# Kernel optimization log

Measured on AMD Instinct MI355X. Metric: run time of the kernel, lower is better.

## Reference

```python
import jax, jax.numpy as jnp
import numpy as np

N_NODES = 50000


def gcn_conv(x, W, b, src, dst, n_nodes):
    """PyG-style GCNConv: self-loops + symmetric deg^-1/2 normalization.

    x: [N, Fin], W: [Fin, Fout], b: [Fout], src/dst: [E] int.
    """
    h = x @ W  # [N, Fout] -- transform before aggregation (small GEMM)
    loop = jnp.arange(n_nodes, dtype=src.dtype)
    src2 = jnp.concatenate([src, loop])  # [E+N]
    dst2 = jnp.concatenate([dst, loop])
    # degree on target nodes (all edge weights = 1, includes self loops)
    deg = jax.ops.segment_sum(jnp.ones(src2.shape[0], dtype=h.dtype), dst2,
                              num_segments=n_nodes)
    dinv = jnp.where(deg > 0, jax.lax.rsqrt(deg), 0.0)
    norm = dinv[src2] * dinv[dst2]  # [E+N]
    msg = h[src2] * norm[:, None]   # gather + scale (memory bound)
    out = jax.ops.segment_sum(msg, dst2, num_segments=n_nodes)  # scatter-add
    return out + b


def setup_inputs() -> dict:
    key = jax.random.key(0)
    ks = jax.random.split(key, 8)
    input_dim, hidden_dim, output_dim = 128, 64, 64
    n_edges = 800000
    x = jax.random.normal(ks[0], (N_NODES, input_dim), dtype=jnp.float32)
    edge_index = jax.random.randint(ks[1], (2, n_edges), 0, N_NODES,
                                    dtype=jnp.int32)
    def glorot(k, fan_in, fan_out):
        s = jnp.sqrt(6.0 / (fan_in + fan_out)).astype(jnp.float32)
        return jax.random.uniform(k, (fan_in, fan_out), jnp.float32, -s, s)
    return {
        "x": x,
        "edge_index": edge_index,
        "W1": glorot(ks[2], input_dim, hidden_dim),
        "b1": jnp.zeros((hidden_dim,), jnp.float32),
        "W2": glorot(ks[3], hidden_dim, output_dim),
        "b2": jnp.zeros((output_dim,), jnp.float32),
        "Wfc": glorot(ks[4], output_dim, 1),
        "bfc": jnp.zeros((1,), jnp.float32),
    }


def reference(x, edge_index, W1, b1, W2, b2, Wfc, bfc):
    src, dst = edge_index[0], edge_index[1]
    h = gcn_conv(x, W1, b1, src, dst, N_NODES)
    h = jax.nn.relu(h)
    h = gcn_conv(h, W2, b2, src, dst, N_NODES)
    logits = h @ Wfc + bfc  # [N, 1]
    return jax.nn.sigmoid(logits)
```

## Files before the change

### kernel.cpp

```cpp
#include <hip/hip_runtime.h>
#include <hip/hip_bf16.h>

#define NN 50000
#define FIN 128
#define NT (NN / 16)
#define NREG 196
#define SLAB 8960
#define NBINB 512
#define CAP2 32
#define NGEMB ((NT + 3) / 4)
#define STCAP 5200

typedef unsigned char u8;
typedef unsigned short u16;
typedef unsigned int u32;
typedef __attribute__((ext_vector_type(8))) short short8;
typedef __attribute__((ext_vector_type(4))) float floatx4;

__device__ __forceinline__ float b2f(u16 v) {
  union { u32 u; float f; } x; x.u = ((u32)v) << 16; return x.f;
}
__device__ __forceinline__ u16 f2b(float f) {
  union { u32 u; float f; } x; x.f = f;
  u32 r = x.u + 0x7FFFu + ((x.u >> 16) & 1u);
  return (u16)(r >> 16);
}
__device__ __forceinline__ float lo16(u32 u) {
  union { u32 x; float f; } c; c.x = u << 16; return c.f;
}
__device__ __forceinline__ float hi16(u32 u) {
  union { u32 x; float f; } c; c.x = u & 0xFFFF0000u; return c.f;
}

__global__ __launch_bounds__(256) void k_prep_bin_gemm(
    const u32* __restrict__ xw, int nxw, const void* __restrict__ w1, int n1w,
    const void* __restrict__ w2, int n2w, const void* __restrict__ wf, int nfw,
    const u16* __restrict__ b2, const u16* __restrict__ bfc,
    float* __restrict__ w2f, float* __restrict__ cbias, int* __restrict__ flags,
    const int* __restrict__ src, const int* __restrict__ dst, int E,
    u32* __restrict__ bucket, u8* __restrict__ cntm,
    const void* __restrict__ X, u16* __restrict__ g,
    float* __restrict__ dinv, float* __restrict__ tvec) {
  int t = threadIdx.x;
  int blk = blockIdx.x;
  if (blk >= NGEMB && blk < NGEMB + NBINB) {
    __shared__ int cnt2[NREG];
    for (int i = t; i < NREG; i += 256) cnt2[i] = 0;
    __syncthreads();
    int sl = blk - NGEMB;
    int lo = (int)((long long)sl * E / NBINB);
    int hi = (int)((long long)(sl + 1) * E / NBINB);
    for (int e = lo + t; e < hi; e += 256) {
      int d = dst[e];
      int s = src[e];
      int r = d >> 8;
      int ofs = atomicAdd(&cnt2[r], 1);
      if (ofs < CAP2)
        bucket[((size_t)sl * NREG + r) * CAP2 + ofs] =
            ((u32)(d & 255) << 16) | (u32)s;
    }
    __syncthreads();
    for (int i = t; i < NREG; i += 256) {
      int c = cnt2[i];
      cntm[(size_t)sl * NREG + i] = (u8)(c > CAP2 ? CAP2 : c);
    }
    return;
  }
  if (blk >= NGEMB + NBINB) {
    __shared__ int sc[3];
    if (t < 3) sc[t] = 0;
    __syncthreads();
    const u32* p2 = (const u32*)w2;
    const u32* pf = (const u32*)wf;
    int n2s = n2w < 1024 ? n2w : 1024;
    int nfs = nfw < 1024 ? nfw : 1024;
    int sn = nxw < 1024 ? nxw : 1024;
    int s2 = 0, sf = 0, sx = 0;
    for (int i = t; i < n2s; i += 256) {
      u32 w = p2[i];
      u32 e = (w >> 7) & 0xFFu;
      s2 += (e >= 100u && e <= 132u) ? 1 : -1;
    }
    for (int i = t; i < nfs; i += 256) {
      u32 w = pf[i];
      u32 e = (w >> 7) & 0xFFu;
      sf += (e >= 100u && e <= 132u) ? 1 : -1;
    }
    for (int i = t; i < sn; i += 256) {
      u32 w = xw[i];
      u32 e = (w >> 7) & 0xFFu;
      sx += (e >= 100u && e <= 132u) ? 1 : -1;
    }
    if (s2) atomicAdd(&sc[0], s2);
    if (sf) atomicAdd(&sc[1], sf);
    if (sx) atomicAdd(&sc[2], sx);
    __syncthreads();
    int f2 = sc[0] > 0, f3 = sc[1] > 0;
    if (t == 0) { flags[0] = sc[2] > 0; flags[2] = f2; flags[3] = f3; }
    if (t < 64) {
      float acc = 0.f;
      for (int j = 0; j < 64; ++j) {
        float w2v = f2 ? b2f(((const u16*)w2)[t * 64 + j])
                       : ((const float*)w2)[t * 64 + j];
        float wfv = f3 ? b2f(((const u16*)wf)[j]) : ((const float*)wf)[j];
        acc += w2v * wfv;
      }
      w2f[t] = acc;
    } else if (t == 64) {
      float acc = b2f(bfc[0]);
      for (int j = 0; j < 64; ++j) {
        float wfv = f3 ? b2f(((const u16*)wf)[j]) : ((const float*)wf)[j];
        acc += b2f(b2[j]) * wfv;
      }
      cbias[0] = acc;
    } else if (t >= 128 && t < 192) {
      g[(size_t)NN * 64 + (t - 128)] = 0;
    } else if (t == 192) {
      tvec[NN] = 0.f;
    } else if (t == 193) {
      dinv[NN] = 0.f;
    }
    return;
  }
  __shared__ u16 lwh[FIN * 64];
  __shared__ u16 lwl[FIN * 64];
  __shared__ int scg[2];
  if (t < 2) scg[t] = 0;
  __syncthreads();
  {
    int sn = nxw < 1024 ? nxw : 1024;
    int sx = 0;
    for (int i = t; i < sn; i += 256) {
      u32 w = xw[i];
      u32 e = (w >> 7) & 0xFFu;
      sx += (e >= 100u && e <= 132u) ? 1 : -1;
    }
    if (sx) atomicAdd(&scg[0], sx);
    int s1n = n1w < 1024 ? n1w : 1024;
    const u32* p1 = (const u32*)w1;
    int s1 = 0;
    for (int i = t; i < s1n; i += 256) {
      u32 w = p1[i];
      u32 e = (w >> 7) & 0xFFu;
      s1 += (e >= 100u && e <= 132u) ? 1 : -1;
    }
    if (s1) atomicAdd(&scg[1], s1);
  }
  __syncthreads();
  bool xb = scg[0] > 0;
  bool w1b = scg[1] > 0;
  for (int i = t; i < FIN * 64; i += 256) {
    int j = i & 7, L = (i >> 3) & 63, f = i >> 9;
    int k = (f >> 2) * 32 + (L >> 4) * 8 + j;
    int n = (f & 3) * 16 + (L & 15);
    int idx = k * 64 + n;
    float v = w1b ? b2f(((const u16*)w1)[idx]) : ((const float*)w1)[idx];
    u16 hb = f2b(v);
    lwh[i] = hb;
    lwl[i] = f2b(v - b2f(hb));
  }
  __syncthreads();
  constexpr int KC = FIN / 32;
  int wave = t >> 6, lane = t & 63;
  int rt = blk * 4 + wave;
  if (rt >= NT) return;
  int m = rt * 16 + (lane & 15);
  int q = (lane >> 4) * 8;
  short8 ah[KC], al[KC];
  if (xb) {
    const u16* xr = (const u16*)X + (size_t)m * FIN + q;
#pragma unroll
    for (int kc = 0; kc < KC; ++kc) ah[kc] = *(const short8*)(xr + kc * 32);
  } else {
    const float* xr = (const float*)X + (size_t)m * FIN + q;
#pragma unroll
    for (int kc = 0; kc < KC; ++kc) {
      float4 v0 = *(const float4*)(xr + kc * 32);
      float4 v1 = *(const float4*)(xr + kc * 32 + 4);
      float v[8] = {v0.x, v0.y, v0.z, v0.w, v1.x, v1.y, v1.z, v1.w};
      short8 h8, l8;
#pragma unroll
      for (int j = 0; j < 8; ++j) {
        u16 hb = f2b(v[j]);
        h8[j] = (short)hb;
        l8[j] = (short)f2b(v[j] - b2f(hb));
      }
      ah[kc] = h8;
      al[kc] = l8;
    }
  }
  int row0 = rt * 16 + (lane >> 4) * 4;
  int c0 = lane & 15;
#pragma unroll
  for (int ct = 0; ct < 4; ++ct) {
    short8 bh[KC], bl[KC];
#pragma unroll
    for (int kc = 0; kc < KC; ++kc) {
      int fo = ((kc * 4 + ct) * 64 + lane) * 8;
      bh[kc] = *(const short8*)(lwh + fo);
      bl[kc] = *(const short8*)(lwl + fo);
    }
    floatx4 acc = (floatx4)(0.f);
#pragma unroll
    for (int kc = 0; kc < KC; ++kc) {
      if (!xb)
        acc = __builtin_amdgcn_mfma_f32_16x16x32_bf16(al[kc], bh[kc], acc, 0, 0, 0);
      acc = __builtin_amdgcn_mfma_f32_16x16x32_bf16(ah[kc], bl[kc], acc, 0, 0, 0);
      acc = __builtin_amdgcn_mfma_f32_16x16x32_bf16(ah[kc], bh[kc], acc, 0, 0, 0);
    }
    size_t o = (size_t)row0 * 64 + ct * 16 + c0;
#pragma unroll
    for (int r = 0; r < 4; ++r) g[o + (size_t)r * 64] = f2b(acc[r]);
  }
}

__global__ __launch_bounds__(512) void k_assemble(
    const u32* __restrict__ bucket, const u8* __restrict__ cntm,
    int* __restrict__ rowstart, int* __restrict__ cnt,
    float* __restrict__ dinv, u16* __restrict__ csr) {
  __shared__ u32 stage[STCAP];
  __shared__ int h[256];
  __shared__ int off[256];
  __shared__ int wsum[8];
  __shared__ int nws[4];
  __shared__ int tot_s;
  int r = blockIdx.x, t = threadIdx.x;
  int lane = t & 63, w = t >> 6;
  int c = (int)cntm[(size_t)t * NREG + r];
  int xv = c;
  for (int d = 1; d < 64; d <<= 1) {
    int y = __shfl_up(xv, d);
    if (lane >= d) xv += y;
  }
  if (lane == 63) wsum[w] = xv;
  if (t < 256) h[t] = 0;
  __syncthreads();
  int add = 0;
  for (int j = 0; j < w; ++j) add += wsum[j];
  int beg = xv + add - c;
  if (t == 0) {
    int tt = 0;
    for (int j = 0; j < 8; ++j) tt += wsum[j];
    tot_s = tt > STCAP ? STCAP : tt;
  }
  const u32* b = bucket + ((size_t)t * NREG + r) * CAP2;
  for (int i = 0; i < c; ++i) {
    int p = beg + i;
    if (p < STCAP) stage[p] = b[i];
  }
  __syncthreads();
  int tot = tot_s;
  for (int i = t; i < tot; i += 512) atomicAdd(&h[stage[i] >> 16], 1);
  __syncthreads();
  int grs = 0, p16 = 0, hc = 0, sv = 0;
  if (t < 256) {
    hc = h[t];
    p16 = (hc + 15) & ~15;
    sv = p16;
    for (int d = 1; d < 64; d <<= 1) {
      int y = __shfl_up(sv, d);
      if (lane >= d) sv += y;
    }
    if (lane == 63) nws[w] = sv;
  }
  __syncthreads();
  if (t < 256) {
    int a2 = 0;
    for (int j = 0; j < w; ++j) a2 += nws[j];
    sv += a2;
    grs = r * SLAB + sv - p16;
    int v = r * 256 + t;
    if (v < NN) {
      rowstart[v] = grs;
      cnt[v] = hc;
      dinv[v] = rsqrtf((float)(hc + 1));
    }
    off[t] = grs;
  }
  __syncthreads();
  for (int i = t; i < tot; i += 512) {
    u32 pk = stage[i];
    int pos = atomicAdd(&off[pk >> 16], 1);
    csr[pos] = (u16)(pk & 0xFFFFu);
  }
  __syncthreads();
  if (t < 256) {
    int v = r * 256 + t;
    if (v < NN) {
      int end = grs + p16;
      for (int pos = off[t]; pos < end; ++pos) csr[pos] = (u16)NN;
    }
  }
}

__global__ __launch_bounds__(256) void k_agg1t(const u32* __restrict__ gu,
                                               const float* __restrict__ dinv,
                                               const int* __restrict__ cnt,
                                               const int* __restrict__ rowstart,
                                               const u16* __restrict__ csr,
                                               const u16* __restrict__ bias,
                                               const float* __restrict__ w2f,
                                               float* __restrict__ tvec) {
  int tid = threadIdx.x;
  int wave = tid >> 6, lane = tid & 63;
  int hf = lane >> 5, c2 = lane & 31;
  int v = (blockIdx.x * 4 + wave) * 4;
  int rs[4], pd[4];
  float dvl[4], a0[4], a1[4];
  int pm = 0;
#pragma unroll
  for (int n = 0; n < 4; ++n) {
    rs[n] = rowstart[v + n];
    int c = cnt[v + n];
    pd[n] = (c + 15) & ~15;
    dvl[n] = dinv[v + n];
    u32 u = gu[(size_t)(v + n) * 32 + c2];
    a0[n] = hf ? 0.f : dvl[n] * lo16(u);
    a1[n] = hf ? 0.f : dvl[n] * hi16(u);
    pm = pd[n] > pm ? pd[n] : pm;
  }
  for (int j = 0; j < pm; j += 16) {
#pragma unroll
    for (int n = 0; n < 4; ++n) {
      if (j < pd[n]) {
        uint4 cw = *(const uint4*)(csr + rs[n] + j + hf * 8);
        u32 idv[8] = {cw.x & 0xFFFFu, cw.x >> 16, cw.y & 0xFFFFu, cw.y >> 16,
                      cw.z & 0xFFFFu, cw.z >> 16, cw.w & 0xFFFFu, cw.w >> 16};
#pragma unroll
        for (int i = 0; i < 8; ++i) {
          u32 u = gu[(size_t)idv[i] * 32 + c2];
          float dvs = dinv[idv[i]];
          a0[n] = fmaf(dvs, lo16(u), a0[n]);
          a1[n] = fmaf(dvs, hi16(u), a1[n]);
        }
      }
    }
  }
  float bv0 = b2f(bias[2 * c2]);
  float bv1 = b2f(bias[2 * c2 + 1]);
  float wf0 = w2f[2 * c2];
  float wf1 = w2f[2 * c2 + 1];
#pragma unroll
  for (int n = 0; n < 4; ++n) {
    float s0 = a0[n] + __shfl_xor(a0[n], 32);
    float s1 = a1[n] + __shfl_xor(a1[n], 32);
    float val = fmaxf(dvl[n] * s0 + bv0, 0.0f) * wf0 +
                fmaxf(dvl[n] * s1 + bv1, 0.0f) * wf1;
    for (int o = 16; o > 0; o >>= 1) val += __shfl_xor(val, o);
    if (lane == n) tvec[v + n] = dvl[n] * val;
  }
}

__global__ __launch_bounds__(256) void k_aggz(const float* __restrict__ tvec,
                                              const float* __restrict__ dinv,
                                              const int* __restrict__ rowstart,
                                              const int* __restrict__ cnt,
                                              const u16* __restrict__ csr,
                                              const float* __restrict__ cbias,
                                              void* __restrict__ out,
                                              const int* __restrict__ flags) {
  int tid = threadIdx.x;
  int wave = tid >> 6, lane = tid & 63;
  int sub = lane >> 4, slot = lane & 15;
  int v = blockIdx.x * 16 + wave * 4 + sub;
  int rs = rowstart[v];
  int pdeg = (cnt[v] + 15) & ~15;
  float acc = 0.f;
  for (int j = slot; j < pdeg; j += 16) acc += tvec[csr[rs + j]];
  for (int o = 8; o > 0; o >>= 1) acc += __shfl_xor(acc, o);
  if (slot == 0) {
    float z = dinv[v] * (acc + tvec[v]) + cbias[0];
    float sg = 1.0f / (1.0f + __expf(-z));
    if (flags[0]) ((u16*)out)[v] = f2b(sg);
    else ((float*)out)[v] = sg;
  }
}

extern "C" void kernel_launch(void* const* d_in, const int* in_sizes, int n_in,
                              void* d_out, int out_size, void* d_ws, size_t ws_size,
                              hipStream_t stream) {
  const void* x = d_in[0];
  const int* ei = (const int*)d_in[1];
  const void* W1 = d_in[2];
  const u16* b1 = (const u16*)d_in[3];
  const void* W2 = d_in[4];
  const u16* b2 = (const u16*)d_in[5];
  const void* Wfc = d_in[6];
  const u16* bfc = (const u16*)d_in[7];

  int E = in_sizes[1] / 2;
  const int* src = ei;
  const int* dst = ei + E;

  char* base = (char*)d_ws;
  size_t off = 0;
  auto alloc = [&](size_t bytes) {
    void* p = base + off;
    off = (off + bytes + 255) & ~(size_t)255;
    return p;
  };
  int* flags = (int*)alloc(8 * 4);
  float* w2f = (float*)alloc(64 * 4);
  float* cbias = (float*)alloc(4);
  int* cnt = (int*)alloc((size_t)NN * 4);
  int* rowstart = (int*)alloc((size_t)NN * 4);
  float* dinv = (float*)alloc((size_t)(NN + 1) * 4);
  u32* bucket = (u32*)alloc((size_t)NBINB * NREG * CAP2 * 4);
  u8* cntm = (u8*)alloc((size_t)NBINB * NREG);
  u16* csr = (u16*)alloc((size_t)NREG * SLAB * 2);
  u16* g = (u16*)alloc((size_t)(NN + 1) * 64 * 2);
  float* tvec = (float*)alloc((size_t)(NN + 1) * 4);

  k_prep_bin_gemm<<<NGEMB + NBINB + 1, 256, 0, stream>>>(
      (const u32*)x, in_sizes[0] / 2, W1, in_sizes[2] / 2, W2, in_sizes[4] / 2,
      Wfc, in_sizes[6] / 2, b2, bfc, w2f, cbias, flags, src, dst, E, bucket,
      cntm, x, g, dinv, tvec);
  k_assemble<<<NREG, 512, 0, stream>>>(bucket, cntm, rowstart, cnt, dinv, csr);
  k_agg1t<<<NN / 16, 256, 0, stream>>>((const u32*)g, dinv, cnt, rowstart, csr,
                                       b1, w2f, tvec);
  k_aggz<<<NN / 16, 256, 0, stream>>>(tvec, dinv, rowstart, cnt, csr, cbias,
                                      d_out, flags);
}
```

Baseline: 142.6 us.

## Prescale GEMM output by source dinv and co-schedule GEMM with CSR assembly

Degree counts are now computed with global atomics during edge binning, so the layer-1 GEMM can multiply each output row by its source dinv before storing. This lets the first aggregation sum pre-scaled rows without gathering dinv per edge. The GEMM blocks move into the same launch as CSR assembly, each with 8 waves, and binning plus weight folding form their own kernel. The cost is 800K global atomics on cnt, an extra memset, and bf16 rounding applied after the scaling, which changes numerics slightly.

New measurement: 169.6 us. 18.9% more time.

```diff
diff --git a/kernel.cpp b/kernel.cpp
--- a/kernel.cpp
+++ b/kernel.cpp
@@ -8,7 +8,7 @@
 #define SLAB 8960
 #define NBINB 512
 #define CAP2 32
-#define NGEMB ((NT + 3) / 4)
+#define NGEMB2 ((NT + 7) / 8)
 #define STCAP 5200
 
 typedef unsigned char u8;
@@ -32,199 +32,207 @@
   union { u32 x; float f; } c; c.x = u & 0xFFFF0000u; return c.f;
 }
 
-__global__ __launch_bounds__(256) void k_prep_bin_gemm(
-    const u32* __restrict__ xw, int nxw, const void* __restrict__ w1, int n1w,
-    const void* __restrict__ w2, int n2w, const void* __restrict__ wf, int nfw,
-    const u16* __restrict__ b2, const u16* __restrict__ bfc,
-    float* __restrict__ w2f, float* __restrict__ cbias, int* __restrict__ flags,
+__global__ __launch_bounds__(256) void k_bin_misc(
+    const u32* __restrict__ xw, int nxw, const void* __restrict__ w2, int n2w,
+    const void* __restrict__ wf, int nfw, const u16* __restrict__ b2,
+    const u16* __restrict__ bfc, float* __restrict__ w2f,
+    float* __restrict__ cbias, int* __restrict__ flags,
     const int* __restrict__ src, const int* __restrict__ dst, int E,
-    u32* __restrict__ bucket, u8* __restrict__ cntm,
-    const void* __restrict__ X, u16* __restrict__ g,
-    float* __restrict__ dinv, float* __restrict__ tvec) {
+    u32* __restrict__ bucket, u8* __restrict__ cntm, int* __restrict__ cnt,
+    u16* __restrict__ g, float* __restrict__ dinv, float* __restrict__ tvec) {
   int t = threadIdx.x;
   int blk = blockIdx.x;
-  if (blk >= NGEMB && blk < NGEMB + NBINB) {
+  if (blk < NBINB) {
     __shared__ int cnt2[NREG];
     for (int i = t; i < NREG; i += 256) cnt2[i] = 0;
     __syncthreads();
-    int sl = blk - NGEMB;
-    int lo = (int)((long long)sl * E / NBINB);
-    int hi = (int)((long long)(sl + 1) * E / NBINB);
+    int lo = (int)((long long)blk * E / NBINB);
+    int hi = (int)((long long)(blk + 1) * E / NBINB);
     for (int e = lo + t; e < hi; e += 256) {
       int d = dst[e];
       int s = src[e];
+      atomicAdd(&cnt[d], 1);
       int r = d >> 8;
       int ofs = atomicAdd(&cnt2[r], 1);
       if (ofs < CAP2)
-        bucket[((size_t)sl * NREG + r) * CAP2 + ofs] =
+        bucket[((size_t)blk * NREG + r) * CAP2 + ofs] =
             ((u32)(d & 255) << 16) | (u32)s;
     }
     __syncthreads();
     for (int i = t; i < NREG; i += 256) {
       int c = cnt2[i];
-      cntm[(size_t)sl * NREG + i] = (u8)(c > CAP2 ? CAP2 : c);
+      cntm[(size_t)blk * NREG + i] = (u8)(c > CAP2 ? CAP2 : c);
     }
     return;
   }
-  if (blk >= NGEMB + NBINB) {
-    __shared__ int sc[3];
-    if (t < 3) sc[t] = 0;
+  __shared__ int sc[3];
+  if (t < 3) sc[t] = 0;
+  __syncthreads();
+  const u32* p2 = (const u32*)w2;
+  const u32* pf = (const u32*)wf;
+  int n2s = n2w < 1024 ? n2w : 1024;
+  int nfs = nfw < 1024 ? nfw : 1024;
+  int sn = nxw < 1024 ? nxw : 1024;
+  int s2 = 0, sf = 0, sx = 0;
+  for (int i = t; i < n2s; i += 256) {
+    u32 w = p2[i];
+    u32 e = (w >> 7) & 0xFFu;
+    s2 += (e >= 100u && e <= 132u) ? 1 : -1;
+  }
+  for (int i = t; i < nfs; i += 256) {
+    u32 w = pf[i];
+    u32 e = (w >> 7) & 0xFFu;
+    sf += (e >= 100u && e <= 132u) ? 1 : -1;
+  }
+  for (int i = t; i < sn; i += 256) {
+    u32 w = xw[i];
+    u32 e = (w >> 7) & 0xFFu;
+    sx += (e >= 100u && e <= 132u) ? 1 : -1;
+  }
+  if (s2) atomicAdd(&sc[0], s2);
+  if (sf) atomicAdd(&sc[1], sf);
+  if (sx) atomicAdd(&sc[2], sx);
+  __syncthreads();
+  int f2 = sc[0] > 0, f3 = sc[1] > 0;
+  if (t == 0) { flags[0] = sc[2] > 0; flags[2] = f2; flags[3] = f3; }
+  if (t < 64) {
+    float acc = 0.f;
+    for (int j = 0; j < 64; ++j) {
+      float w2v = f2 ? b2f(((const u16*)w2)[t * 64 + j])
+                     : ((const float*)w2)[t * 64 + j];
+      float wfv = f3 ? b2f(((const u16*)wf)[j]) : ((const float*)wf)[j];
+      acc += w2v * wfv;
+    }
+    w2f[t] = acc;
+  } else if (t == 64) {
+    float acc = b2f(bfc[0]);
+    for (int j = 0; j < 64; ++j) {
+      float wfv = f3 ? b2f(((const u16*)wf)[j]) : ((const float*)wf)[j];
+      acc += b2f(b2[j]) * wfv;
+    }
+    cbias[0] = acc;
+  } else if (t >= 128 && t < 192) {
+    g[(size_t)NN * 64 + (t - 128)] = 0;
+  } else if (t == 192) {
+    tvec[NN] = 0.f;
+  } else if (t == 193) {
+    dinv[NN] = 0.f;
+  }
+}
+
+__global__ __launch_bounds__(512) void k_gemm_assemble(
+    const u32* __restrict__ xw, int nxw, const void* __restrict__ w1, int n1w,
+    const void* __restrict__ X, const int* __restrict__ cnt,
+    const u32* __restrict__ bucket, const u8* __restrict__ cntm,
+    int* __restrict__ rowstart, float* __restrict__ dinv,
+    u16* __restrict__ csr, u16* __restrict__ g) {
+  __shared__ u32 smemu[8448];
+  int t = threadIdx.x;
+  int blk = blockIdx.x;
+  if (blk < NGEMB2) {
+    u16* lwh = (u16*)smemu;
+    u16* lwl = (u16*)(smemu + 4096);
+    int* scg = (int*)(smemu + 8192);
+    if (t < 2) scg[t] = 0;
     __syncthreads();
-    const u32* p2 = (const u32*)w2;
-    const u32* pf = (const u32*)wf;
-    int n2s = n2w < 1024 ? n2w : 1024;
-    int nfs = nfw < 1024 ? nfw : 1024;
-    int sn = nxw < 1024 ? nxw : 1024;
-    int s2 = 0, sf = 0, sx = 0;
-    for (int i = t; i < n2s; i += 256) {
-      u32 w = p2[i];
-      u32 e = (w >> 7) & 0xFFu;
-      s2 += (e >= 100u && e <= 132u) ? 1 : -1;
-    }
-    for (int i = t; i < nfs; i += 256) {
-      u32 w = pf[i];
-      u32 e = (w >> 7) & 0xFFu;
-      sf += (e >= 100u && e <= 132u) ? 1 : -1;
-    }
-    for (int i = t; i < sn; i += 256) {
-      u32 w = xw[i];
-      u32 e = (w >> 7) & 0xFFu;
-      sx += (e >= 100u && e <= 132u) ? 1 : -1;
-    }
-    if (s2) atomicAdd(&sc[0], s2);
-    if (sf) atomicAdd(&sc[1], sf);
-    if (sx) atomicAdd(&sc[2], sx);
+    {
+      int sn = nxw < 1024 ? nxw : 1024;
+      int sx = 0;
+      for (int i = t; i < sn; i += 512) {
+        u32 w = xw[i];
+        u32 e = (w >> 7) & 0xFFu;
+        sx += (e >= 100u && e <= 132u) ? 1 : -1;
+      }
+      if (sx) atomicAdd(&scg[0], sx);
+      int s1n = n1w < 1024 ? n1w : 1024;
+      const u32* p1 = (const u32*)w1;
+      int s1 = 0;
+      for (int i = t; i < s1n; i += 512) {
+        u32 w = p1[i];
+        u32 e = (w >> 7) & 0xFFu;
+        s1 += (e >= 100u && e <= 132u) ? 1 : -1;
+      }
+      if (s1) atomicAdd(&scg[1], s1);
+    }
     __syncthreads();
-    int f2 = sc[0] > 0, f3 = sc[1] > 0;
-    if (t == 0) { flags[0] = sc[2] > 0; flags[2] = f2; flags[3] = f3; }
-    if (t < 64) {
-      float acc = 0.f;
-      for (int j = 0; j < 64; ++j) {
-        float w2v = f2 ? b2f(((const u16*)w2)[t * 64 + j])
-                       : ((const float*)w2)[t * 64 + j];
-        float wfv = f3 ? b2f(((const u16*)wf)[j]) : ((const float*)wf)[j];
-        acc += w2v * wfv;
-      }
-      w2f[t] = acc;
-    } else if (t == 64) {
-      float acc = b2f(bfc[0]);
-      for (int j = 0; j < 64; ++j) {
-        float wfv = f3 ? b2f(((const u16*)wf)[j]) : ((const float*)wf)[j];
-        acc += b2f(b2[j]) * wfv;
-      }
-      cbias[0] = acc;
-    } else if (t >= 128 && t < 192) {
-      g[(size_t)NN * 64 + (t - 128)] = 0;
-    } else if (t == 192) {
-      tvec[NN] = 0.f;
-    } else if (t == 193) {
-      dinv[NN] = 0.f;
+    bool xb = scg[0] > 0;
+    bool w1b = scg[1] > 0;
+    for (int i = t; i < FIN * 64; i += 512) {
+      int j = i & 7, L = (i >> 3) & 63, f = i >> 9;
+      int k = (f >> 2) * 32 + (L >> 4) * 8 + j;
+      int n = (f & 3) * 16 + (L & 15);
+      int idx = k * 64 + n;
+      float v = w1b ? b2f(((const u16*)w1)[idx]) : ((const float*)w1)[idx];
+      u16 hb = f2b(v);
+      lwh[i] = hb;
+      lwl[i] = f2b(v - b2f(hb));
+    }
+    __syncthreads();
+    constexpr int KC = FIN / 32;
+    int wave = t >> 6, lane = t & 63;
+    int rt = blk * 8 + wave;
+    if (rt >= NT) return;
+    int m = rt * 16 + (lane & 15);
+    int q = (lane >> 4) * 8;
+    short8 ah[KC], al[KC];
+    if (xb) {
+      const u16* xr = (const u16*)X + (size_t)m * FIN + q;
+#pragma unroll
+      for (int kc = 0; kc < KC; ++kc) ah[kc] = *(const short8*)(xr + kc * 32);
+    } else {
+      const float* xr = (const float*)X + (size_t)m * FIN + q;
+#pragma unroll
+      for (int kc = 0; kc < KC; ++kc) {
+        float4 v0 = *(const float4*)(xr + kc * 32);
+        float4 v1 = *(const float4*)(xr + kc * 32 + 4);
+        float v[8] = {v0.x, v0.y, v0.z, v0.w, v1.x, v1.y, v1.z, v1.w};
+        short8 h8, l8;
+#pragma unroll
+        for (int j = 0; j < 8; ++j) {
+          u16 hb = f2b(v[j]);
+          h8[j] = (short)hb;
+          l8[j] = (short)f2b(v[j] - b2f(hb));
+        }
+        ah[kc] = h8;
+        al[kc] = l8;
+      }
+    }
+    int row0 = rt * 16 + (lane >> 4) * 4;
+    int c0 = lane & 15;
+    float dvr[4];
+#pragma unroll
+    for (int r = 0; r < 4; ++r)
+      dvr[r] = rsqrtf((float)(cnt[row0 + r] + 1));
+#pragma unroll
+    for (int ct = 0; ct < 4; ++ct) {
+      short8 bh[KC], bl[KC];
+#pragma unroll
+      for (int kc = 0; kc < KC; ++kc) {
+        int fo = ((kc * 4 + ct) * 64 + lane) * 8;
+        bh[kc] = *(const short8*)(lwh + fo);
+        bl[kc] = *(const short8*)(lwl + fo);
+      }
+      floatx4 acc = (floatx4)(0.f);
+#pragma unroll
+      for (int kc = 0; kc < KC; ++kc) {
+        if (!xb)
+          acc = __builtin_amdgcn_mfma_f32_16x16x32_bf16(al[kc], bh[kc], acc, 0, 0, 0);
+        acc = __builtin_amdgcn_mfma_f32_16x16x32_bf16(ah[kc], bl[kc], acc, 0, 0, 0);
+        acc = __builtin_amdgcn_mfma_f32_16x16x32_bf16(ah[kc], bh[kc], acc, 0, 0, 0);
+      }
+      size_t o = (size_t)row0 * 64 + ct * 16 + c0;
+#pragma unroll
+      for (int r = 0; r < 4; ++r) g[o + (size_t)r * 64] = f2b(acc[r] * dvr[r]);
     }
     return;
   }
-  __shared__ u16 lwh[FIN * 64];
-  __shared__ u16 lwl[FIN * 64];
-  __shared__ int scg[2];
-  if (t < 2) scg[t] = 0;
-  __syncthreads();
-  {
-    int sn = nxw < 1024 ? nxw : 1024;
-    int sx = 0;
-    for (int i = t; i < sn; i += 256) {
-      u32 w = xw[i];
-      u32 e = (w >> 7) & 0xFFu;
-      sx += (e >= 100u && e <= 132u) ? 1 : -1;
-    }
-    if (sx) atomicAdd(&scg[0], sx);
-    int s1n = n1w < 1024 ? n1w : 1024;
-    const u32* p1 = (const u32*)w1;
-    int s1 = 0;
-    for (int i = t; i < s1n; i += 256) {
-      u32 w = p1[i];
-      u32 e = (w >> 7) & 0xFFu;
-      s1 += (e >= 100u && e <= 132u) ? 1 : -1;
-    }
-    if (s1) atomicAdd(&scg[1], s1);
-  }
-  __syncthreads();
-  bool xb = scg[0] > 0;
-  bool w1b = scg[1] > 0;
-  for (int i = t; i < FIN * 64; i += 256) {
-    int j = i & 7, L = (i >> 3) & 63, f = i >> 9;
-    int k = (f >> 2) * 32 + (L >> 4) * 8 + j;
-    int n = (f & 3) * 16 + (L & 15);
-    int idx = k * 64 + n;
-    float v = w1b ? b2f(((const u16*)w1)[idx]) : ((const float*)w1)[idx];
-    u16 hb = f2b(v);
-    lwh[i] = hb;
-    lwl[i] = f2b(v - b2f(hb));
-  }
-  __syncthreads();
-  constexpr int KC = FIN / 32;
-  int wave = t >> 6, lane = t & 63;
-  int rt = blk * 4 + wave;
-  if (rt >= NT) return;
-  int m = rt * 16 + (lane & 15);
-  int q = (lane >> 4) * 8;
-  short8 ah[KC], al[KC];
-  if (xb) {
-    const u16* xr = (const u16*)X + (size_t)m * FIN + q;
-#pragma unroll
-    for (int kc = 0; kc < KC; ++kc) ah[kc] = *(const short8*)(xr + kc * 32);
-  } else {
-    const float* xr = (const float*)X + (size_t)m * FIN + q;
-#pragma unroll
-    for (int kc = 0; kc < KC; ++kc) {
-      float4 v0 = *(const float4*)(xr + kc * 32);
-      float4 v1 = *(const float4*)(xr + kc * 32 + 4);
-      float v[8] = {v0.x, v0.y, v0.z, v0.w, v1.x, v1.y, v1.z, v1.w};
-      short8 h8, l8;
-#pragma unroll
-      for (int j = 0; j < 8; ++j) {
-        u16 hb = f2b(v[j]);
-        h8[j] = (short)hb;
-        l8[j] = (short)f2b(v[j] - b2f(hb));
-      }
-      ah[kc] = h8;
-      al[kc] = l8;
-    }
-  }
-  int row0 = rt * 16 + (lane >> 4) * 4;
-  int c0 = lane & 15;
-#pragma unroll
-  for (int ct = 0; ct < 4; ++ct) {
-    short8 bh[KC], bl[KC];
-#pragma unroll
-    for (int kc = 0; kc < KC; ++kc) {
-      int fo = ((kc * 4 + ct) * 64 + lane) * 8;
-      bh[kc] = *(const short8*)(lwh + fo);
-      bl[kc] = *(const short8*)(lwl + fo);
-    }
-    floatx4 acc = (floatx4)(0.f);
-#pragma unroll
-    for (int kc = 0; kc < KC; ++kc) {
-      if (!xb)
-        acc = __builtin_amdgcn_mfma_f32_16x16x32_bf16(al[kc], bh[kc], acc, 0, 0, 0);
-      acc = __builtin_amdgcn_mfma_f32_16x16x32_bf16(ah[kc], bl[kc], acc, 0, 0, 0);
-      acc = __builtin_amdgcn_mfma_f32_16x16x32_bf16(ah[kc], bh[kc], acc, 0, 0, 0);
-    }
-    size_t o = (size_t)row0 * 64 + ct * 16 + c0;
-#pragma unroll
-    for (int r = 0; r < 4; ++r) g[o + (size_t)r * 64] = f2b(acc[r]);
-  }
-}
-
-__global__ __launch_bounds__(512) void k_assemble(
-    const u32* __restrict__ bucket, const u8* __restrict__ cntm,
-    int* __restrict__ rowstart, int* __restrict__ cnt,
-    float* __restrict__ dinv, u16* __restrict__ csr) {
-  __shared__ u32 stage[STCAP];
-  __shared__ int h[256];
-  __shared__ int off[256];
-  __shared__ int wsum[8];
-  __shared__ int nws[4];
-  __shared__ int tot_s;
-  int r = blockIdx.x, t = threadIdx.x;
+  u32* stage = smemu;
+  int* h = (int*)(smemu + 5200);
+  int* off = (int*)(smemu + 5456);
+  int* wsum = (int*)(smemu + 5712);
+  int* nws = (int*)(smemu + 5720);
+  int* tot_s = (int*)(smemu + 5724);
+  int r = blk - NGEMB2;
   int lane = t & 63, w = t >> 6;
   int c = (int)cntm[(size_t)t * NREG + r];
   int xv = c;
@@ -241,7 +249,7 @@
   if (t == 0) {
     int tt = 0;
     for (int j = 0; j < 8; ++j) tt += wsum[j];
-    tot_s = tt > STCAP ? STCAP : tt;
+    tot_s[0] = tt > STCAP ? STCAP : tt;
   }
   const u32* b = bucket + ((size_t)t * NREG + r) * CAP2;
   for (int i = 0; i < c; ++i) {
@@ -249,7 +257,7 @@
     if (p < STCAP) stage[p] = b[i];
   }
   __syncthreads();
-  int tot = tot_s;
+  int tot = tot_s[0];
   for (int i = t; i < tot; i += 512) atomicAdd(&h[stage[i] >> 16], 1);
   __syncthreads();
   int grs = 0, p16 = 0, hc = 0, sv = 0;
@@ -272,7 +280,6 @@
     int v = r * 256 + t;
     if (v < NN) {
       rowstart[v] = grs;
-      cnt[v] = hc;
       dinv[v] = rsqrtf((float)(hc + 1));
     }
     off[t] = grs;
@@ -315,8 +322,8 @@
     pd[n] = (c + 15) & ~15;
     dvl[n] = dinv[v + n];
     u32 u = gu[(size_t)(v + n) * 32 + c2];
-    a0[n] = hf ? 0.f : dvl[n] * lo16(u);
-    a1[n] = hf ? 0.f : dvl[n] * hi16(u);
+    a0[n] = hf ? 0.f : lo16(u);
+    a1[n] = hf ? 0.f : hi16(u);
     pm = pd[n] > pm ? pd[n] : pm;
   }
   for (int j = 0; j < pm; j += 16) {
@@ -329,9 +336,8 @@
 #pragma unroll
         for (int i = 0; i < 8; ++i) {
           u32 u = gu[(size_t)idv[i] * 32 + c2];
-          float dvs = dinv[idv[i]];
-          a0[n] = fmaf(dvs, lo16(u), a0[n]);
-          a1[n] = fmaf(dvs, hi16(u), a1[n]);
+          a0[n] += lo16(u);
+          a1[n] += hi16(u);
         }
       }
     }
@@ -411,11 +417,14 @@
   u16* g = (u16*)alloc((size_t)(NN + 1) * 64 * 2);
   float* tvec = (float*)alloc((size_t)(NN + 1) * 4);
 
-  k_prep_bin_gemm<<<NGEMB + NBINB + 1, 256, 0, stream>>>(
-      (const u32*)x, in_sizes[0] / 2, W1, in_sizes[2] / 2, W2, in_sizes[4] / 2,
-      Wfc, in_sizes[6] / 2, b2, bfc, w2f, cbias, flags, src, dst, E, bucket,
-      cntm, x, g, dinv, tvec);
-  k_assemble<<<NREG, 512, 0, stream>>>(bucket, cntm, rowstart, cnt, dinv, csr);
+  hipMemsetAsync(cnt, 0, (size_t)NN * 4, stream);
+  k_bin_misc<<<NBINB + 1, 256, 0, stream>>>(
+      (const u32*)x, in_sizes[0] / 2, W2, in_sizes[4] / 2, Wfc,
+      in_sizes[6] / 2, b2, bfc, w2f, cbias, flags, src, dst, E, bucket, cntm,
+      cnt, g, dinv, tvec);
+  k_gemm_assemble<<<NGEMB2 + NREG, 512, 0, stream>>>(
+      (const u32*)x, in_sizes[0] / 2, W1, in_sizes[2] / 2, x, cnt, bucket,
+      cntm, rowstart, dinv, csr, g);
   k_agg1t<<<NN / 16, 256, 0, stream>>>((const u32*)g, dinv, cnt, rowstart, csr,
                                        b1, w2f, tvec);
   k_aggz<<<NN / 16, 256, 0, stream>>>(tvec, dinv, rowstart, cnt, csr, cbias,
```

## Prescale GEMM output by dinv in assemble, drop per-edge dinv gathers

Applied to the files above, without the earlier changes.

The first kernel now runs 512-thread blocks covering 8 row tiles each, sharing one LDS union buffer. The low-part weight MFMA is skipped when W1 is already bf16. The assemble kernel multiplies each row of g by its own deg^-1/2 in place, so the layer-1 aggregation no longer gathers dinv per edge. That removes one random load per edge in the hot loop, but adds a read-modify-write pass over g and a second bf16 rounding of the scaled features.

Result: no change. 144.7 us (+1.4%).

```diff
diff --git a/kernel.cpp b/kernel.cpp
--- a/kernel.cpp
+++ b/kernel.cpp
@@ -8,7 +8,7 @@
 #define SLAB 8960
 #define NBINB 512
 #define CAP2 32
-#define NGEMB ((NT + 3) / 4)
+#define NGEMB2 ((NT + 7) / 8)
 #define STCAP 5200
 
 typedef unsigned char u8;
@@ -32,7 +32,7 @@
   union { u32 x; float f; } c; c.x = u & 0xFFFF0000u; return c.f;
 }
 
-__global__ __launch_bounds__(256) void k_prep_bin_gemm(
+__global__ __launch_bounds__(512) void k_gemm_bin_misc(
     const u32* __restrict__ xw, int nxw, const void* __restrict__ w1, int n1w,
     const void* __restrict__ w2, int n2w, const void* __restrict__ wf, int nfw,
     const u16* __restrict__ b2, const u16* __restrict__ bfc,
@@ -41,16 +41,17 @@
     u32* __restrict__ bucket, u8* __restrict__ cntm,
     const void* __restrict__ X, u16* __restrict__ g,
     float* __restrict__ dinv, float* __restrict__ tvec) {
+  __shared__ u32 smemu[8448];
   int t = threadIdx.x;
   int blk = blockIdx.x;
-  if (blk >= NGEMB && blk < NGEMB + NBINB) {
-    __shared__ int cnt2[NREG];
-    for (int i = t; i < NREG; i += 256) cnt2[i] = 0;
+  if (blk >= NGEMB2 && blk < NGEMB2 + NBINB) {
+    int* cnt2 = (int*)smemu;
+    for (int i = t; i < NREG; i += 512) cnt2[i] = 0;
     __syncthreads();
-    int sl = blk - NGEMB;
+    int sl = blk - NGEMB2;
     int lo = (int)((long long)sl * E / NBINB);
     int hi = (int)((long long)(sl + 1) * E / NBINB);
-    for (int e = lo + t; e < hi; e += 256) {
+    for (int e = lo + t; e < hi; e += 512) {
       int d = dst[e];
       int s = src[e];
       int r = d >> 8;
@@ -60,14 +61,14 @@
             ((u32)(d & 255) << 16) | (u32)s;
     }
     __syncthreads();
-    for (int i = t; i < NREG; i += 256) {
+    for (int i = t; i < NREG; i += 512) {
       int c = cnt2[i];
       cntm[(size_t)sl * NREG + i] = (u8)(c > CAP2 ? CAP2 : c);
     }
     return;
   }
-  if (blk >= NGEMB + NBINB) {
-    __shared__ int sc[3];
+  if (blk >= NGEMB2 + NBINB) {
+    int* sc = (int*)smemu;
     if (t < 3) sc[t] = 0;
     __syncthreads();
     const u32* p2 = (const u32*)w2;
@@ -76,17 +77,17 @@
     int nfs = nfw < 1024 ? nfw : 1024;
     int sn = nxw < 1024 ? nxw : 1024;
     int s2 = 0, sf = 0, sx = 0;
-    for (int i = t; i < n2s; i += 256) {
+    for (int i = t; i < n2s; i += 512) {
       u32 w = p2[i];
       u32 e = (w >> 7) & 0xFFu;
       s2 += (e >= 100u && e <= 132u) ? 1 : -1;
     }
-    for (int i = t; i < nfs; i += 256) {
+    for (int i = t; i < nfs; i += 512) {
       u32 w = pf[i];
       u32 e = (w >> 7) & 0xFFu;
       sf += (e >= 100u && e <= 132u) ? 1 : -1;
     }
-    for (int i = t; i < sn; i += 256) {
+    for (int i = t; i < sn; i += 512) {
       u32 w = xw[i];
       u32 e = (w >> 7) & 0xFFu;
       sx += (e >= 100u && e <= 132u) ? 1 : -1;
@@ -122,15 +123,15 @@
     }
     return;
   }
-  __shared__ u16 lwh[FIN * 64];
-  __shared__ u16 lwl[FIN * 64];
-  __shared__ int scg[2];
+  u16* lwh = (u16*)smemu;
+  u16* lwl = (u16*)(smemu + 4096);
+  int* scg = (int*)(smemu + 8192);
   if (t < 2) scg[t] = 0;
   __syncthreads();
   {
     int sn = nxw < 1024 ? nxw : 1024;
     int sx = 0;
-    for (int i = t; i < sn; i += 256) {
+    for (int i = t; i < sn; i += 512) {
       u32 w = xw[i];
       u32 e = (w >> 7) & 0xFFu;
       sx += (e >= 100u && e <= 132u) ? 1 : -1;
@@ -139,7 +140,7 @@
     int s1n = n1w < 1024 ? n1w : 1024;
     const u32* p1 = (const u32*)w1;
     int s1 = 0;
-    for (int i = t; i < s1n; i += 256) {
+    for (int i = t; i < s1n; i += 512) {
       u32 w = p1[i];
       u32 e = (w >> 7) & 0xFFu;
       s1 += (e >= 100u && e <= 132u) ? 1 : -1;
@@ -149,7 +150,7 @@
   __syncthreads();
   bool xb = scg[0] > 0;
   bool w1b = scg[1] > 0;
-  for (int i = t; i < FIN * 64; i += 256) {
+  for (int i = t; i < FIN * 64; i += 512) {
     int j = i & 7, L = (i >> 3) & 63, f = i >> 9;
     int k = (f >> 2) * 32 + (L >> 4) * 8 + j;
     int n = (f & 3) * 16 + (L & 15);
@@ -162,7 +163,7 @@
   __syncthreads();
   constexpr int KC = FIN / 32;
   int wave = t >> 6, lane = t & 63;
-  int rt = blk * 4 + wave;
+  int rt = blk * 8 + wave;
   if (rt >= NT) return;
   int m = rt * 16 + (lane & 15);
   int q = (lane >> 4) * 8;
@@ -193,19 +194,21 @@
   int c0 = lane & 15;
 #pragma unroll
   for (int ct = 0; ct < 4; ++ct) {
-    short8 bh[KC], bl[KC];
+    short8 bh[KC];
 #pragma unroll
     for (int kc = 0; kc < KC; ++kc) {
       int fo = ((kc * 4 + ct) * 64 + lane) * 8;
       bh[kc] = *(const short8*)(lwh + fo);
-      bl[kc] = *(const short8*)(lwl + fo);
     }
     floatx4 acc = (floatx4)(0.f);
 #pragma unroll
     for (int kc = 0; kc < KC; ++kc) {
       if (!xb)
         acc = __builtin_amdgcn_mfma_f32_16x16x32_bf16(al[kc], bh[kc], acc, 0, 0, 0);
-      acc = __builtin_amdgcn_mfma_f32_16x16x32_bf16(ah[kc], bl[kc], acc, 0, 0, 0);
+      if (!w1b) {
+        short8 bl = *(const short8*)(lwl + ((kc * 4 + ct) * 64 + lane) * 8);
+        acc = __builtin_amdgcn_mfma_f32_16x16x32_bf16(ah[kc], bl, acc, 0, 0, 0);
+      }
       acc = __builtin_amdgcn_mfma_f32_16x16x32_bf16(ah[kc], bh[kc], acc, 0, 0, 0);
     }
     size_t o = (size_t)row0 * 64 + ct * 16 + c0;
@@ -214,10 +217,10 @@
   }
 }
 
-__global__ __launch_bounds__(512) void k_assemble(
+__global__ __launch_bounds__(512) void k_assemble_scale(
     const u32* __restrict__ bucket, const u8* __restrict__ cntm,
     int* __restrict__ rowstart, int* __restrict__ cnt,
-    float* __restrict__ dinv, u16* __restrict__ csr) {
+    float* __restrict__ dinv, u16* __restrict__ csr, u16* __restrict__ g) {
   __shared__ u32 stage[STCAP];
   __shared__ int h[256];
   __shared__ int off[256];
@@ -289,6 +292,25 @@
     if (v < NN) {
       int end = grs + p16;
       for (int pos = off[t]; pos < end; ++pos) csr[pos] = (u16)NN;
+    }
+  }
+  {
+    int row = r * 256 + (t >> 1);
+    if (row < NN) {
+      float dv = rsqrtf((float)(h[t >> 1] + 1));
+      u32* gp = (u32*)g + (size_t)row * 32 + (t & 1) * 16;
+#pragma unroll
+      for (int k2 = 0; k2 < 4; ++k2) {
+        uint4 a = *(uint4*)(gp + k2 * 4);
+        u32 o[4] = {a.x, a.y, a.z, a.w};
+#pragma unroll
+        for (int j = 0; j < 4; ++j) {
+          u32 lw = (u32)f2b(dv * lo16(o[j]));
+          u32 hw = (u32)f2b(dv * hi16(o[j]));
+          o[j] = lw | (hw << 16);
+        }
+        *(uint4*)(gp + k2 * 4) = make_uint4(o[0], o[1], o[2], o[3]);
+      }
     }
   }
 }
@@ -315,8 +337,8 @@
     pd[n] = (c + 15) & ~15;
     dvl[n] = dinv[v + n];
     u32 u = gu[(size_t)(v + n) * 32 + c2];
-    a0[n] = hf ? 0.f : dvl[n] * lo16(u);
-    a1[n] = hf ? 0.f : dvl[n] * hi16(u);
+    a0[n] = hf ? 0.f : lo16(u);
+    a1[n] = hf ? 0.f : hi16(u);
     pm = pd[n] > pm ? pd[n] : pm;
   }
   for (int j = 0; j < pm; j += 16) {
@@ -329,9 +351,8 @@
 #pragma unroll
         for (int i = 0; i < 8; ++i) {
           u32 u = gu[(size_t)idv[i] * 32 + c2];
-          float dvs = dinv[idv[i]];
-          a0[n] = fmaf(dvs, lo16(u), a0[n]);
-          a1[n] = fmaf(dvs, hi16(u), a1[n]);
+          a0[n] += lo16(u);
+          a1[n] += hi16(u);
         }
       }
     }
@@ -411,11 +432,12 @@
   u16* g = (u16*)alloc((size_t)(NN + 1) * 64 * 2);
   float* tvec = (float*)alloc((size_t)(NN + 1) * 4);
 
-  k_prep_bin_gemm<<<NGEMB + NBINB + 1, 256, 0, stream>>>(
+  k_gemm_bin_misc<<<NGEMB2 + NBINB + 1, 512, 0, stream>>>(
       (const u32*)x, in_sizes[0] / 2, W1, in_sizes[2] / 2, W2, in_sizes[4] / 2,
       Wfc, in_sizes[6] / 2, b2, bfc, w2f, cbias, flags, src, dst, E, bucket,
       cntm, x, g, dinv, tvec);
-  k_assemble<<<NREG, 512, 0, stream>>>(bucket, cntm, rowstart, cnt, dinv, csr);
+  k_assemble_scale<<<NREG, 512, 0, stream>>>(bucket, cntm, rowstart, cnt, dinv,
+                                             csr, g);
   k_agg1t<<<NN / 16, 256, 0, stream>>>((const u32*)g, dinv, cnt, rowstart, csr,
                                        b1, w2f, tvec);
   k_aggz<<<NN / 16, 256, 0, stream>>>(tvec, dinv, rowstart, cnt, csr, cbias,
```
